# Performance work log

Measured on AMD Instinct MI355X. Metric: run time of the kernel, lower is better.

The kernel has to match this reference:

```python
import jax, jax.numpy as jnp
import numpy as np

N = 100000      # nodes
E = 1600000     # edges (avg degree 16)
F_IN = 128
F_HID = 128
LN_EPS = 1e-5


def setup_inputs() -> dict:
    key = jax.random.key(0)
    ks = jax.random.split(key, 4)
    x = jax.random.normal(ks[0], (N, F_IN), dtype=jnp.float32)
    edge_index = jax.random.randint(ks[1], (2, E), 0, N, dtype=jnp.int32)
    W1 = jax.random.normal(ks[2], (F_IN, F_HID), dtype=jnp.float32) * 0.05
    W2 = jax.random.normal(ks[3], (F_HID, F_HID), dtype=jnp.float32) * 0.05
    return {
        "x": x,
        "edge_index": edge_index,
        "W1": W1, "b1": jnp.zeros((F_HID,), jnp.float32),
        "W2": W2, "b2": jnp.zeros((F_HID,), jnp.float32),
        "g1": jnp.ones((F_HID,), jnp.float32), "be1": jnp.zeros((F_HID,), jnp.float32),
        "g2": jnp.ones((F_HID,), jnp.float32), "be2": jnp.zeros((F_HID,), jnp.float32),
    }


def layer_norm(x, gamma, beta):
    mu = jnp.mean(x, axis=-1, keepdims=True)
    var = jnp.mean(jnp.square(x - mu), axis=-1, keepdims=True)
    return (x - mu) * jax.lax.rsqrt(var + LN_EPS) * gamma + beta


def gcn_conv(x, src, dst, W, b):
    """PyG GCNConv: linear transform, add self-loops, symmetric-normalized scatter-add."""
    n = x.shape[0]
    loop = jnp.arange(n, dtype=src.dtype)
    s = jnp.concatenate([src, loop])   # [E+N] sources (incl. self-loops)
    d = jnp.concatenate([dst, loop])   # [E+N] destinations
    deg = jax.ops.segment_sum(jnp.ones(s.shape[0], x.dtype), d, num_segments=n)
    dinv = jnp.where(deg > 0, jax.lax.rsqrt(deg), 0.0)
    norm = dinv[s] * dinv[d]           # [E+N] edge normalization
    h = x @ W                          # [N, F_hid] transform BEFORE propagate (PyG order)
    msg = h[s] * norm[:, None]         # [E+N, F_hid] gathered, normalized messages
    out = jax.ops.segment_sum(msg, d, num_segments=n)
    return out + b


def reference(x, edge_index, W1, b1, W2, b2, g1, be1, g2, be2):
    # GCN_body, layer=2, layer_norm_first=False, use_ln=True, eval mode (dropout=identity)
    src, dst = edge_index[0], edge_index[1]
    h = layer_norm(jax.nn.relu(gcn_conv(x, src, dst, W1, b1)), g1, be1)
    h = layer_norm(jax.nn.relu(gcn_conv(h, src, dst, W2, b2)), g2, be2)
    return h
```

## Files before the change

### kernel.cpp

```cpp
#include <hip/hip_runtime.h>

#define FDIM 128
#define LN_EPS 1e-5f

typedef short short8 __attribute__((ext_vector_type(8)));
typedef float f32x4 __attribute__((ext_vector_type(4)));

__device__ __forceinline__ ushort f2bf(float f) {
    uint u = __float_as_uint(f);
    u += 0x7fff + ((u >> 16) & 1);
    return (ushort)(u >> 16);
}
__device__ __forceinline__ float bflo(uint u) { return __uint_as_float(u << 16); }
__device__ __forceinline__ float bfhi(uint u) { return __uint_as_float(u & 0xffff0000u); }

__global__ void k_count(const int* __restrict__ dst, int* __restrict__ cnt,
                        ushort* __restrict__ pos, int E) {
    int e = blockIdx.x * 256 + threadIdx.x;
    if (e < E) pos[e] = (ushort)atomicAdd(&cnt[dst[e]], 1);
}

__global__ __launch_bounds__(1024) void k_scan_block(const int* __restrict__ cnt,
                                                     int* __restrict__ rowptr,
                                                     int* __restrict__ partial, int N) {
    __shared__ int s[1024];
    int t = threadIdx.x;
    int i = blockIdx.x * 1024 + t;
    int v = (i < N) ? ((cnt[i] + 7) & ~7) : 0;
    s[t] = v;
    __syncthreads();
    for (int off = 1; off < 1024; off <<= 1) {
        int u = (t >= off) ? s[t - off] : 0;
        __syncthreads();
        s[t] += u;
        __syncthreads();
    }
    if (i < N) rowptr[i] = s[t] - v;
    if (t == 1023) partial[blockIdx.x] = s[1023];
}

__global__ __launch_bounds__(1024) void k_scan_partial(int* __restrict__ partial, int NB) {
    __shared__ int s[1024];
    int t = threadIdx.x;
    int v = (t < NB) ? partial[t] : 0;
    s[t] = v;
    __syncthreads();
    for (int off = 1; off < 1024; off <<= 1) {
        int u = (t >= off) ? s[t - off] : 0;
        __syncthreads();
        s[t] += u;
        __syncthreads();
    }
    if (t < NB) partial[t] = s[t] - v;
}

__global__ void k_finalize(int* __restrict__ rowptr, const int* __restrict__ partial,
                           const int* __restrict__ cnt, float* __restrict__ dinv,
                           int* __restrict__ col, int N, int E) {
    int i = blockIdx.x * 256 + threadIdx.x;
    if (i < N) {
        int rp = rowptr[i] + partial[i >> 10];
        rowptr[i] = rp;
        int deg = cnt[i];
        int deg8 = (deg + 7) & ~7;
        dinv[i] = rsqrtf((float)deg + 1.0f);
        for (int k = deg; k < deg8; ++k) col[rp + k] = N;
        if (i == N - 1) rowptr[N] = rp + deg8;
    }
}

__global__ void k_wt2(const float* __restrict__ W1, const float* __restrict__ W2,
                      ushort* __restrict__ WT1, ushort* __restrict__ WT2) {
    int b = blockIdx.x, k = threadIdx.x;
    if (b < 128) WT1[b * 128 + k] = f2bf(W1[k * 128 + b]);
    else         WT2[(b - 128) * 128 + k] = f2bf(W2[k * 128 + (b - 128)]);
}

template <bool F32IN>
__device__ __forceinline__ void gemm_body(char* sXb, char* sWb,
                                          const void* __restrict__ Xin,
                                          const ushort* __restrict__ WT,
                                          const float* __restrict__ dinv,
                                          ushort* __restrict__ H, int N, int bid) {
    int t = threadIdx.x;
    int w = t >> 6, lane = t & 63;
    int cl = lane & 15, kq = lane >> 4;
    int base = bid * 64;

    const short8* Wg = (const short8*)WT;
#pragma unroll
    for (int k = 0; k < 8; ++k) {
        int idx = t + k * 256;
        int c = idx >> 4, ch = idx & 15;
        *(short8*)(sWb + c * 256 + ((ch * 16) ^ ((c & 7) << 4))) = Wg[idx];
    }

    if constexpr (F32IN) {
        const float4* X4 = (const float4*)Xin;
        size_t lim = (size_t)N * 32 - 1;
#pragma unroll
        for (int k = 0; k < 8; ++k) {
            int idx = t + k * 256;
            size_t gi = (size_t)base * 32 + idx;
            float4 v = X4[gi < lim ? gi : lim];
            ushort4 o;
            o.x = f2bf(v.x); o.y = f2bf(v.y); o.z = f2bf(v.z); o.w = f2bf(v.w);
            int row = idx >> 5, b8 = (idx & 31) * 8;
            *(ushort4*)(sXb + row * 256 + (b8 ^ ((row & 7) << 4))) = o;
        }
    } else {
        const short8* X8 = (const short8*)Xin;
        size_t lim = (size_t)N * 16 - 1;
#pragma unroll
        for (int k = 0; k < 4; ++k) {
            int idx = t + k * 256;
            size_t gi = (size_t)base * 16 + idx;
            short8 v = X8[gi < lim ? gi : lim];
            int row = idx >> 4, b16 = (idx & 15) * 16;
            *(short8*)(sXb + row * 256 + (b16 ^ ((row & 7) << 4))) = v;
        }
    }
    __syncthreads();

    int rl = w * 16 + cl;
    short8 b0, b1, b2, b3;
#pragma unroll
    for (int kt = 0; kt < 4; ++kt) {
        short8 v = *(const short8*)(sXb + rl * 256 + ((kt * 64 + kq * 16) ^ ((rl & 7) << 4)));
        if (kt == 0) b0 = v; else if (kt == 1) b1 = v; else if (kt == 2) b2 = v; else b3 = v;
    }

    int r = base + rl;
    bool ok = r < N;
    float di = dinv[min(r, N - 1)];
#pragma unroll
    for (int nt = 0; nt < 8; ++nt) {
        int c = nt * 16 + cl;
        int sw = (c & 7) << 4;
        f32x4 acc = {0.f, 0.f, 0.f, 0.f};
        acc = __builtin_amdgcn_mfma_f32_16x16x32_bf16(
            *(const short8*)(sWb + c * 256 + ((0 * 64 + kq * 16) ^ sw)), b0, acc, 0, 0, 0);
        acc = __builtin_amdgcn_mfma_f32_16x16x32_bf16(
            *(const short8*)(sWb + c * 256 + ((1 * 64 + kq * 16) ^ sw)), b1, acc, 0, 0, 0);
        acc = __builtin_amdgcn_mfma_f32_16x16x32_bf16(
            *(const short8*)(sWb + c * 256 + ((2 * 64 + kq * 16) ^ sw)), b2, acc, 0, 0, 0);
        acc = __builtin_amdgcn_mfma_f32_16x16x32_bf16(
            *(const short8*)(sWb + c * 256 + ((3 * 64 + kq * 16) ^ sw)), b3, acc, 0, 0, 0);
        if (ok) {
            ushort4 o;
            o.x = f2bf(acc[0] * di); o.y = f2bf(acc[1] * di);
            o.z = f2bf(acc[2] * di); o.w = f2bf(acc[3] * di);
            *(ushort4*)(H + (size_t)r * 128 + nt * 16 + kq * 4) = o;
        }
    }
}

template <bool F32IN>
__global__ __launch_bounds__(256) void k_gemm(const void* __restrict__ Xin,
                                              const ushort* __restrict__ WT,
                                              const float* __restrict__ dinv,
                                              ushort* __restrict__ H, int N) {
    __shared__ ushort sX[64 * 128];
    __shared__ ushort sW[128 * 128];
    gemm_body<F32IN>((char*)sX, (char*)sW, Xin, WT, dinv, H, N, blockIdx.x);
}

__global__ __launch_bounds__(256) void k_mega(const void* __restrict__ Xin,
                                              const ushort* __restrict__ WT,
                                              const float* __restrict__ dinv,
                                              ushort* __restrict__ H, int N, int ngemm,
                                              const int* __restrict__ src,
                                              const int* __restrict__ dst,
                                              const int* __restrict__ rowptr,
                                              const ushort* __restrict__ pos,
                                              int* __restrict__ col, int E) {
    __shared__ ushort sX[64 * 128];
    __shared__ ushort sW[128 * 128];
    if (blockIdx.x < (uint)ngemm) {
        gemm_body<true>((char*)sX, (char*)sW, Xin, WT, dinv, H, N, blockIdx.x);
    } else {
        int e = (blockIdx.x - ngemm) * 256 + threadIdx.x;
        if (e < E) col[rowptr[dst[e]] + (int)pos[e]] = src[e];
    }
}

__global__ __launch_bounds__(256) void k_agg(const uint4* __restrict__ H4,
                                             const int* __restrict__ rowptr,
                                             const int* __restrict__ col,
                                             const float* __restrict__ dinv,
                                             const float* __restrict__ bias,
                                             const float* __restrict__ gamma,
                                             const float* __restrict__ beta,
                                             float* __restrict__ outf,
                                             uint4* __restrict__ outb,
                                             int N) {
    int wave = threadIdx.x >> 6;
    int lane = threadIdx.x & 63;
    int q = lane >> 4;
    int l = lane & 15;
    int node = blockIdx.x * 16 + wave * 4 + q;
    bool valid = node < N;
    int nodec = valid ? node : N - 1;

    float di = dinv[nodec];
    uint4 hs = H4[(uint)nodec * 16u + (uint)l];
    float a0 = bflo(hs.x), a1 = bfhi(hs.x), a2 = bflo(hs.y), a3 = bfhi(hs.y);
    float a4 = bflo(hs.z), a5 = bfhi(hs.z), a6 = bflo(hs.w), a7 = bfhi(hs.w);

    int beg = rowptr[nodec];
    int deg8 = rowptr[nodec + 1] - beg;
    const int* cp = col + beg;

    for (int i = 0; i < deg8; i += 8) {
        int s0 = cp[i + 0], s1 = cp[i + 1], s2 = cp[i + 2], s3 = cp[i + 3];
        int s4 = cp[i + 4], s5 = cp[i + 5], s6 = cp[i + 6], s7 = cp[i + 7];
        uint4 u0 = H4[(uint)s0 * 16u + (uint)l];
        uint4 u1 = H4[(uint)s1 * 16u + (uint)l];
        uint4 u2 = H4[(uint)s2 * 16u + (uint)l];
        uint4 u3 = H4[(uint)s3 * 16u + (uint)l];
        uint4 u4 = H4[(uint)s4 * 16u + (uint)l];
        uint4 u5 = H4[(uint)s5 * 16u + (uint)l];
        uint4 u6 = H4[(uint)s6 * 16u + (uint)l];
        uint4 u7 = H4[(uint)s7 * 16u + (uint)l];
        a0 += bflo(u0.x); a1 += bfhi(u0.x); a2 += bflo(u0.y); a3 += bfhi(u0.y);
        a4 += bflo(u0.z); a5 += bfhi(u0.z); a6 += bflo(u0.w); a7 += bfhi(u0.w);
        a0 += bflo(u1.x); a1 += bfhi(u1.x); a2 += bflo(u1.y); a3 += bfhi(u1.y);
        a4 += bflo(u1.z); a5 += bfhi(u1.z); a6 += bflo(u1.w); a7 += bfhi(u1.w);
        a0 += bflo(u2.x); a1 += bfhi(u2.x); a2 += bflo(u2.y); a3 += bfhi(u2.y);
        a4 += bflo(u2.z); a5 += bfhi(u2.z); a6 += bflo(u2.w); a7 += bfhi(u2.w);
        a0 += bflo(u3.x); a1 += bfhi(u3.x); a2 += bflo(u3.y); a3 += bfhi(u3.y);
        a4 += bflo(u3.z); a5 += bfhi(u3.z); a6 += bflo(u3.w); a7 += bfhi(u3.w);
        a0 += bflo(u4.x); a1 += bfhi(u4.x); a2 += bflo(u4.y); a3 += bfhi(u4.y);
        a4 += bflo(u4.z); a5 += bfhi(u4.z); a6 += bflo(u4.w); a7 += bfhi(u4.w);
        a0 += bflo(u5.x); a1 += bfhi(u5.x); a2 += bflo(u5.y); a3 += bfhi(u5.y);
        a4 += bflo(u5.z); a5 += bfhi(u5.z); a6 += bflo(u5.w); a7 += bfhi(u5.w);
        a0 += bflo(u6.x); a1 += bfhi(u6.x); a2 += bflo(u6.y); a3 += bfhi(u6.y);
        a4 += bflo(u6.z); a5 += bfhi(u6.z); a6 += bflo(u6.w); a7 += bfhi(u6.w);
        a0 += bflo(u7.x); a1 += bfhi(u7.x); a2 += bflo(u7.y); a3 += bfhi(u7.y);
        a4 += bflo(u7.z); a5 += bfhi(u7.z); a6 += bflo(u7.w); a7 += bfhi(u7.w);
    }

    float4 bb0 = ((const float4*)bias)[2 * l];
    float4 bb1 = ((const float4*)bias)[2 * l + 1];
    a0 = fmaxf(fmaf(a0, di, bb0.x), 0.f);
    a1 = fmaxf(fmaf(a1, di, bb0.y), 0.f);
    a2 = fmaxf(fmaf(a2, di, bb0.z), 0.f);
    a3 = fmaxf(fmaf(a3, di, bb0.w), 0.f);
    a4 = fmaxf(fmaf(a4, di, bb1.x), 0.f);
    a5 = fmaxf(fmaf(a5, di, bb1.y), 0.f);
    a6 = fmaxf(fmaf(a6, di, bb1.z), 0.f);
    a7 = fmaxf(fmaf(a7, di, bb1.w), 0.f);

    float s1 = ((a0 + a1) + (a2 + a3)) + ((a4 + a5) + (a6 + a7));
    float s2 = ((a0 * a0 + a1 * a1) + (a2 * a2 + a3 * a3)) +
               ((a4 * a4 + a5 * a5) + (a6 * a6 + a7 * a7));
#pragma unroll
    for (int off = 8; off >= 1; off >>= 1) {
        s1 += __shfl_xor(s1, off);
        s2 += __shfl_xor(s2, off);
    }
    float mu = s1 * (1.f / 128.f);
    float var = s2 * (1.f / 128.f) - mu * mu;
    float rs = rsqrtf(var + LN_EPS);

    float4 g0 = ((const float4*)gamma)[2 * l];
    float4 g1 = ((const float4*)gamma)[2 * l + 1];
    float4 e0 = ((const float4*)beta)[2 * l];
    float4 e1 = ((const float4*)beta)[2 * l + 1];
    float o0 = (a0 - mu) * rs * g0.x + e0.x;
    float o1 = (a1 - mu) * rs * g0.y + e0.y;
    float o2 = (a2 - mu) * rs * g0.z + e0.z;
    float o3 = (a3 - mu) * rs * g0.w + e0.w;
    float o4 = (a4 - mu) * rs * g1.x + e1.x;
    float o5 = (a5 - mu) * rs * g1.y + e1.y;
    float o6 = (a6 - mu) * rs * g1.z + e1.z;
    float o7 = (a7 - mu) * rs * g1.w + e1.w;

    if (!valid) return;
    if (outf) {
        ((float4*)outf)[(size_t)node * 32 + 2 * l]     = make_float4(o0, o1, o2, o3);
        ((float4*)outf)[(size_t)node * 32 + 2 * l + 1] = make_float4(o4, o5, o6, o7);
    } else {
        uint4 o;
        o.x = (uint)f2bf(o0) | ((uint)f2bf(o1) << 16);
        o.y = (uint)f2bf(o2) | ((uint)f2bf(o3) << 16);
        o.z = (uint)f2bf(o4) | ((uint)f2bf(o5) << 16);
        o.w = (uint)f2bf(o6) | ((uint)f2bf(o7) << 16);
        outb[(size_t)node * 16 + l] = o;
    }
}

extern "C" void kernel_launch(void* const* d_in, const int* in_sizes, int n_in,
                              void* d_out, int out_size, void* d_ws, size_t ws_size,
                              hipStream_t stream) {
    const float* x  = (const float*)d_in[0];
    const int*   ei = (const int*)d_in[1];
    const float* W1 = (const float*)d_in[2];
    const float* b1 = (const float*)d_in[3];
    const float* W2 = (const float*)d_in[4];
    const float* b2 = (const float*)d_in[5];
    const float* g1 = (const float*)d_in[6];
    const float* be1 = (const float*)d_in[7];
    const float* g2 = (const float*)d_in[8];
    const float* be2 = (const float*)d_in[9];

    int N = in_sizes[0] / FDIM;
    int E = in_sizes[1] / 2;
    const int* srcp = ei;
    const int* dstp = ei + E;
    float* out = (float*)d_out;

    char* w = (char*)d_ws;
    size_t off = 0;
    auto take = [&](size_t bytes) {
        void* p = w + off;
        off = (off + bytes + 255) & ~(size_t)255;
        return p;
    };
    ushort* hb   = (ushort*)take((size_t)(N + 1) * FDIM * sizeof(ushort));
    ushort* WT1  = (ushort*)take(128 * 128 * sizeof(ushort));
    ushort* WT2  = (ushort*)take(128 * 128 * sizeof(ushort));
    int* cnt     = (int*)take((size_t)N * sizeof(int));
    int* rowptr  = (int*)take((size_t)(N + 1) * sizeof(int));
    ushort* pos  = (ushort*)take((size_t)E * sizeof(ushort));
    int* colb    = (int*)take((size_t)(E + 7 * (size_t)N + 8) * sizeof(int));
    float* dinv  = (float*)take((size_t)N * sizeof(float));
    int* partial = (int*)take(1024 * sizeof(int));
    (void)ws_size;

    int NB = (N + 1023) >> 10;
    int ngemm = (N + 63) / 64;
    int nfill = (E + 255) / 256;

    hipMemsetAsync(cnt, 0, (size_t)N * sizeof(int), stream);
    hipMemsetAsync(hb + (size_t)N * FDIM, 0, FDIM * sizeof(ushort), stream);

    k_wt2<<<256, 128, 0, stream>>>(W1, W2, WT1, WT2);

    k_count<<<(E + 255) / 256, 256, 0, stream>>>(dstp, cnt, pos, E);
    k_scan_block<<<NB, 1024, 0, stream>>>(cnt, rowptr, partial, N);
    k_scan_partial<<<1, 1024, 0, stream>>>(partial, NB);
    k_finalize<<<(N + 255) / 256, 256, 0, stream>>>(rowptr, partial, cnt, dinv, colb, N, E);

    k_mega<<<ngemm + nfill, 256, 0, stream>>>(x, WT1, dinv, hb, N, ngemm,
                                              srcp, dstp, rowptr, pos, colb, E);

    k_agg<<<(N + 15) / 16, 256, 0, stream>>>((const uint4*)hb, rowptr, colb, dinv,
                                             b1, g1, be1, nullptr, (uint4*)d_out, N);
    k_gemm<false><<<ngemm, 256, 0, stream>>>(d_out, WT2, dinv, hb, N);
    k_agg<<<(N + 15) / 16, 256, 0, stream>>>((const uint4*)hb, rowptr, colb, dinv,
                                             b2, g2, be2, out, nullptr, N);
}
```

Before: 260.6 us.

## Privatize degree counting per XCD to avoid cross-die atomic contention

```diff
diff --git a/kernel.cpp b/kernel.cpp
--- a/kernel.cpp
+++ b/kernel.cpp
@@ -2,6 +2,7 @@
 
 #define FDIM 128
 #define LN_EPS 1e-5f
+#define NXCD 8
 
 typedef short short8 __attribute__((ext_vector_type(8)));
 typedef float f32x4 __attribute__((ext_vector_type(4)));
@@ -14,19 +15,36 @@
 __device__ __forceinline__ float bflo(uint u) { return __uint_as_float(u << 16); }
 __device__ __forceinline__ float bfhi(uint u) { return __uint_as_float(u & 0xffff0000u); }
 
-__global__ void k_count(const int* __restrict__ dst, int* __restrict__ cnt,
-                        ushort* __restrict__ pos, int E) {
+__device__ __forceinline__ uint xcc_id() {
+    uint x;
+    asm volatile("s_getreg_b32 %0, hwreg(20, 0, 32)" : "=s"(x));
+    return x & (NXCD - 1);
+}
+
+__global__ void k_count(const int* __restrict__ dst, uint* __restrict__ partial,
+                        ushort* __restrict__ pos, int N, int E) {
     int e = blockIdx.x * 256 + threadIdx.x;
-    if (e < E) pos[e] = (ushort)atomicAdd(&cnt[dst[e]], 1);
-}
-
-__global__ __launch_bounds__(1024) void k_scan_block(const int* __restrict__ cnt,
+    uint x = xcc_id();
+    if (e < E) {
+        uint slot = __hip_atomic_fetch_add(&partial[(size_t)x * N + dst[e]], 1u,
+                                           __ATOMIC_RELAXED, __HIP_MEMORY_SCOPE_WORKGROUP);
+        pos[e] = (ushort)((x << 13) | (slot & 0x1FFFu));
+    }
+}
+
+__global__ __launch_bounds__(1024) void k_scan_block(const uint* __restrict__ partial,
                                                      int* __restrict__ rowptr,
-                                                     int* __restrict__ partial, int N) {
+                                                     int* __restrict__ partialscan, int N) {
     __shared__ int s[1024];
     int t = threadIdx.x;
     int i = blockIdx.x * 1024 + t;
-    int v = (i < N) ? ((cnt[i] + 7) & ~7) : 0;
+    int v = 0;
+    if (i < N) {
+        int deg = 0;
+#pragma unroll
+        for (int x = 0; x < NXCD; ++x) deg += (int)partial[(size_t)x * N + i];
+        v = (deg + 7) & ~7;
+    }
     s[t] = v;
     __syncthreads();
     for (int off = 1; off < 1024; off <<= 1) {
@@ -36,13 +54,13 @@
         __syncthreads();
     }
     if (i < N) rowptr[i] = s[t] - v;
-    if (t == 1023) partial[blockIdx.x] = s[1023];
-}
-
-__global__ __launch_bounds__(1024) void k_scan_partial(int* __restrict__ partial, int NB) {
+    if (t == 1023) partialscan[blockIdx.x] = s[1023];
+}
+
+__global__ __launch_bounds__(1024) void k_scan_partial(int* __restrict__ partialscan, int NB) {
     __shared__ int s[1024];
     int t = threadIdx.x;
-    int v = (t < NB) ? partial[t] : 0;
+    int v = (t < NB) ? partialscan[t] : 0;
     s[t] = v;
     __syncthreads();
     for (int off = 1; off < 1024; off <<= 1) {
@@ -51,17 +69,24 @@
         s[t] += u;
         __syncthreads();
     }
-    if (t < NB) partial[t] = s[t] - v;
-}
-
-__global__ void k_finalize(int* __restrict__ rowptr, const int* __restrict__ partial,
-                           const int* __restrict__ cnt, float* __restrict__ dinv,
+    if (t < NB) partialscan[t] = s[t] - v;
+}
+
+__global__ void k_finalize(int* __restrict__ rowptr, const int* __restrict__ partialscan,
+                           uint* __restrict__ partial, float* __restrict__ dinv,
                            int* __restrict__ col, int N, int E) {
     int i = blockIdx.x * 256 + threadIdx.x;
     if (i < N) {
-        int rp = rowptr[i] + partial[i >> 10];
+        int rp = rowptr[i] + partialscan[i >> 10];
         rowptr[i] = rp;
-        int deg = cnt[i];
+        int run = rp, deg = 0;
+#pragma unroll
+        for (int x = 0; x < NXCD; ++x) {
+            uint c = partial[(size_t)x * N + i];
+            partial[(size_t)x * N + i] = (uint)run;
+            run += (int)c;
+            deg += (int)c;
+        }
         int deg8 = (deg + 7) & ~7;
         dinv[i] = rsqrtf((float)deg + 1.0f);
         for (int k = deg; k < deg8; ++k) col[rp + k] = N;
@@ -171,7 +196,7 @@
                                               ushort* __restrict__ H, int N, int ngemm,
                                               const int* __restrict__ src,
                                               const int* __restrict__ dst,
-                                              const int* __restrict__ rowptr,
+                                              const uint* __restrict__ basep,
                                               const ushort* __restrict__ pos,
                                               int* __restrict__ col, int E) {
     __shared__ ushort sX[64 * 128];
@@ -180,7 +205,12 @@
         gemm_body<true>((char*)sX, (char*)sW, Xin, WT, dinv, H, N, blockIdx.x);
     } else {
         int e = (blockIdx.x - ngemm) * 256 + threadIdx.x;
-        if (e < E) col[rowptr[dst[e]] + (int)pos[e]] = src[e];
+        if (e < E) {
+            int d = dst[e];
+            uint u = pos[e];
+            uint x = u >> 13, p = u & 0x1FFFu;
+            col[basep[(size_t)x * N + d] + p] = src[e];
+        }
     }
 }
 
@@ -317,33 +347,33 @@
         off = (off + bytes + 255) & ~(size_t)255;
         return p;
     };
-    ushort* hb   = (ushort*)take((size_t)(N + 1) * FDIM * sizeof(ushort));
-    ushort* WT1  = (ushort*)take(128 * 128 * sizeof(ushort));
-    ushort* WT2  = (ushort*)take(128 * 128 * sizeof(ushort));
-    int* cnt     = (int*)take((size_t)N * sizeof(int));
-    int* rowptr  = (int*)take((size_t)(N + 1) * sizeof(int));
-    ushort* pos  = (ushort*)take((size_t)E * sizeof(ushort));
-    int* colb    = (int*)take((size_t)(E + 7 * (size_t)N + 8) * sizeof(int));
-    float* dinv  = (float*)take((size_t)N * sizeof(float));
-    int* partial = (int*)take(1024 * sizeof(int));
+    ushort* hb    = (ushort*)take((size_t)(N + 1) * FDIM * sizeof(ushort));
+    ushort* WT1   = (ushort*)take(128 * 128 * sizeof(ushort));
+    ushort* WT2   = (ushort*)take(128 * 128 * sizeof(ushort));
+    uint* partial = (uint*)take((size_t)NXCD * N * sizeof(uint));
+    int* rowptr   = (int*)take((size_t)(N + 1) * sizeof(int));
+    ushort* pos   = (ushort*)take((size_t)E * sizeof(ushort));
+    int* colb     = (int*)take((size_t)(E + 7 * (size_t)N + 1024) * sizeof(int));
+    float* dinv   = (float*)take((size_t)N * sizeof(float));
+    int* pscan    = (int*)take(1024 * sizeof(int));
     (void)ws_size;
 
     int NB = (N + 1023) >> 10;
     int ngemm = (N + 63) / 64;
     int nfill = (E + 255) / 256;
 
-    hipMemsetAsync(cnt, 0, (size_t)N * sizeof(int), stream);
+    hipMemsetAsync(partial, 0, (size_t)NXCD * N * sizeof(uint), stream);
     hipMemsetAsync(hb + (size_t)N * FDIM, 0, FDIM * sizeof(ushort), stream);
 
     k_wt2<<<256, 128, 0, stream>>>(W1, W2, WT1, WT2);
 
-    k_count<<<(E + 255) / 256, 256, 0, stream>>>(dstp, cnt, pos, E);
-    k_scan_block<<<NB, 1024, 0, stream>>>(cnt, rowptr, partial, N);
-    k_scan_partial<<<1, 1024, 0, stream>>>(partial, NB);
-    k_finalize<<<(N + 255) / 256, 256, 0, stream>>>(rowptr, partial, cnt, dinv, colb, N, E);
+    k_count<<<(E + 255) / 256, 256, 0, stream>>>(dstp, partial, pos, N, E);
+    k_scan_block<<<NB, 1024, 0, stream>>>(partial, rowptr, pscan, N);
+    k_scan_partial<<<1, 1024, 0, stream>>>(pscan, NB);
+    k_finalize<<<(N + 255) / 256, 256, 0, stream>>>(rowptr, pscan, partial, dinv, colb, N, E);
 
     k_mega<<<ngemm + nfill, 256, 0, stream>>>(x, WT1, dinv, hb, N, ngemm,
-                                              srcp, dstp, rowptr, pos, colb, E);
+                                              srcp, dstp, partial, pos, colb, E);
 
     k_agg<<<(N + 15) / 16, 256, 0, stream>>>((const uint4*)hb, rowptr, colb, dinv,
                                              b1, g1, be1, nullptr, (uint4*)d_out, N);
```

New measurement: 260.5 us. About the same (-0.0%).

## Build CSR with two-level bucketed radix scatter instead of global atomics

Applied to the files above, without the earlier changes.

```diff
diff --git a/kernel.cpp b/kernel.cpp
--- a/kernel.cpp
+++ b/kernel.cpp
@@ -2,6 +2,8 @@
 
 #define FDIM 128
 #define LN_EPS 1e-5f
+#define BSH 9
+#define EPB 2048
 
 typedef short short8 __attribute__((ext_vector_type(8)));
 typedef float f32x4 __attribute__((ext_vector_type(4)));
@@ -14,58 +16,175 @@
 __device__ __forceinline__ float bflo(uint u) { return __uint_as_float(u << 16); }
 __device__ __forceinline__ float bfhi(uint u) { return __uint_as_float(u & 0xffff0000u); }
 
-__global__ void k_count(const int* __restrict__ dst, int* __restrict__ cnt,
-                        ushort* __restrict__ pos, int E) {
-    int e = blockIdx.x * 256 + threadIdx.x;
-    if (e < E) pos[e] = (ushort)atomicAdd(&cnt[dst[e]], 1);
-}
-
-__global__ __launch_bounds__(1024) void k_scan_block(const int* __restrict__ cnt,
-                                                     int* __restrict__ rowptr,
-                                                     int* __restrict__ partial, int N) {
-    __shared__ int s[1024];
+
+__global__ __launch_bounds__(256) void k_bcount(const int* __restrict__ dst,
+                                                uint* __restrict__ mat, int nbk, int E) {
+    __shared__ uint cnt[512];
     int t = threadIdx.x;
-    int i = blockIdx.x * 1024 + t;
-    int v = (i < N) ? ((cnt[i] + 7) & ~7) : 0;
-    s[t] = v;
-    __syncthreads();
-    for (int off = 1; off < 1024; off <<= 1) {
-        int u = (t >= off) ? s[t - off] : 0;
-        __syncthreads();
-        s[t] += u;
-        __syncthreads();
-    }
-    if (i < N) rowptr[i] = s[t] - v;
-    if (t == 1023) partial[blockIdx.x] = s[1023];
-}
-
-__global__ __launch_bounds__(1024) void k_scan_partial(int* __restrict__ partial, int NB) {
-    __shared__ int s[1024];
+    for (int i = t; i < nbk; i += 256) cnt[i] = 0;
+    __syncthreads();
+    int base = blockIdx.x * EPB, end = min(base + EPB, E);
+    for (int e = base + t; e < end; e += 256)
+        atomicAdd(&cnt[(uint)dst[e] >> BSH], 1u);
+    __syncthreads();
+    for (int i = t; i < nbk; i += 256) mat[(size_t)blockIdx.x * nbk + i] = cnt[i];
+}
+
+__global__ __launch_bounds__(1024) void k_colscan(uint* __restrict__ mat,
+                                                  uint* __restrict__ btot, int nbk, int nblk) {
+    __shared__ uint s[1024];
+    int b = blockIdx.x, t = threadIdx.x;
+    uint run = 0;
+    for (int base = 0; base < nblk; base += 1024) {
+        int i = base + t;
+        uint v = (i < nblk) ? mat[(size_t)i * nbk + b] : 0;
+        s[t] = v;
+        __syncthreads();
+        for (int off = 1; off < 1024; off <<= 1) {
+            uint u = (t >= off) ? s[t - off] : 0;
+            __syncthreads();
+            s[t] += u;
+            __syncthreads();
+        }
+        if (i < nblk) mat[(size_t)i * nbk + b] = run + s[t] - v;
+        run += s[1023];
+        __syncthreads();
+    }
+    if (t == 0) btot[b] = run;
+}
+
+__global__ __launch_bounds__(256) void k_bscatter(const int* __restrict__ src,
+                                                  const int* __restrict__ dst,
+                                                  const uint* __restrict__ mat,
+                                                  const uint* __restrict__ btot,
+                                                  uint* __restrict__ ebuf, int nbk, int E) {
+    __shared__ uint cur[512];
+    __shared__ uint ps[256];
     int t = threadIdx.x;
-    int v = (t < NB) ? partial[t] : 0;
-    s[t] = v;
-    __syncthreads();
-    for (int off = 1; off < 1024; off <<= 1) {
-        int u = (t >= off) ? s[t - off] : 0;
-        __syncthreads();
-        s[t] += u;
-        __syncthreads();
-    }
-    if (t < NB) partial[t] = s[t] - v;
-}
-
-__global__ void k_finalize(int* __restrict__ rowptr, const int* __restrict__ partial,
-                           const int* __restrict__ cnt, float* __restrict__ dinv,
-                           int* __restrict__ col, int N, int E) {
-    int i = blockIdx.x * 256 + threadIdx.x;
-    if (i < N) {
-        int rp = rowptr[i] + partial[i >> 10];
-        rowptr[i] = rp;
-        int deg = cnt[i];
-        int deg8 = (deg + 7) & ~7;
-        dinv[i] = rsqrtf((float)deg + 1.0f);
-        for (int k = deg; k < deg8; ++k) col[rp + k] = N;
-        if (i == N - 1) rowptr[N] = rp + deg8;
+    uint v = (t < nbk) ? btot[t] : 0;
+    ps[t] = v;
+    __syncthreads();
+    for (int off = 1; off < 256; off <<= 1) {
+        uint u = (t >= off) ? ps[t - off] : 0;
+        __syncthreads();
+        ps[t] += u;
+        __syncthreads();
+    }
+    if (t < nbk) cur[t] = (ps[t] - v) + mat[(size_t)blockIdx.x * nbk + t];
+    __syncthreads();
+    int base = blockIdx.x * EPB, end = min(base + EPB, E);
+    for (int e = base + t; e < end; e += 256) {
+        uint d = (uint)dst[e];
+        uint off = atomicAdd(&cur[d >> BSH], 1u);
+        ebuf[off] = ((d & 511u) << 17) | (uint)src[e];
+    }
+}
+
+__global__ __launch_bounds__(256) void k_bdeg(const uint* __restrict__ ebuf,
+                                              const uint* __restrict__ btot,
+                                              int* __restrict__ deg, float* __restrict__ dinv,
+                                              uint* __restrict__ padtot, int N, int nbk) {
+    __shared__ uint cnt[512];
+    __shared__ uint ps[256];
+    __shared__ uint begs;
+    int b = blockIdx.x, t = threadIdx.x;
+    for (int i = t; i < 512; i += 256) cnt[i] = 0;
+    uint v = (t < nbk) ? btot[t] : 0;
+    ps[t] = v;
+    __syncthreads();
+    for (int off = 1; off < 256; off <<= 1) {
+        uint u = (t >= off) ? ps[t - off] : 0;
+        __syncthreads();
+        ps[t] += u;
+        __syncthreads();
+    }
+    if (t == b) begs = ps[t] - v;
+    __syncthreads();
+    uint beg = begs, cn = btot[b];
+    for (uint i = t; i < cn; i += 256) atomicAdd(&cnt[ebuf[beg + i] >> 17], 1u);
+    __syncthreads();
+    int n0 = b << BSH;
+    uint loc = 0;
+    for (int i = t; i < 512; i += 256) {
+        int n = n0 + i;
+        if (n < N) {
+            uint dg = cnt[i];
+            deg[n] = (int)dg;
+            dinv[n] = rsqrtf((float)dg + 1.0f);
+            loc += (dg + 7u) & ~7u;
+        }
+    }
+    ps[t] = loc;
+    __syncthreads();
+    for (int off = 128; off >= 1; off >>= 1) {
+        if (t < off) ps[t] += ps[t + off];
+        __syncthreads();
+    }
+    if (t == 0) padtot[b] = ps[0];
+}
+
+__device__ __forceinline__ void bfill_body(const uint* __restrict__ ebuf,
+                                           const uint* __restrict__ btot,
+                                           const uint* __restrict__ padtot,
+                                           const int* __restrict__ deg,
+                                           int* __restrict__ rowptr, int* __restrict__ col,
+                                           int N, int nbk, int b) {
+    __shared__ uint ps[256];
+    __shared__ uint lrp[512];
+    __shared__ uint curf[512];
+    __shared__ uint sc0, sc1;
+    int t = threadIdx.x;
+    uint v = (t < nbk) ? btot[t] : 0;
+    ps[t] = v;
+    __syncthreads();
+    for (int off = 1; off < 256; off <<= 1) {
+        uint u = (t >= off) ? ps[t - off] : 0;
+        __syncthreads();
+        ps[t] += u;
+        __syncthreads();
+    }
+    if (t == b) sc0 = ps[t] - v;
+    __syncthreads();
+    uint w = (t < nbk) ? padtot[t] : 0;
+    ps[t] = w;
+    __syncthreads();
+    for (int off = 1; off < 256; off <<= 1) {
+        uint u = (t >= off) ? ps[t - off] : 0;
+        __syncthreads();
+        ps[t] += u;
+        __syncthreads();
+    }
+    if (t == b) sc1 = ps[t] - w;
+    if (b == nbk - 1 && t == nbk - 1) rowptr[N] = (int)ps[t];
+    __syncthreads();
+    uint beg = sc0, cn = btot[b], base = sc1;
+    int n0 = b << BSH;
+    int nA = n0 + 2 * t, nB = nA + 1;
+    uint dA = (nA < N) ? (uint)deg[nA] : 0;
+    uint dB = (nB < N) ? (uint)deg[nB] : 0;
+    uint pA = (dA + 7u) & ~7u, pB = (dB + 7u) & ~7u;
+    uint pair = pA + pB;
+    ps[t] = pair;
+    __syncthreads();
+    for (int off = 1; off < 256; off <<= 1) {
+        uint u = (t >= off) ? ps[t - off] : 0;
+        __syncthreads();
+        ps[t] += u;
+        __syncthreads();
+    }
+    uint pex = ps[t] - pair;
+    uint rA = base + pex, rB = rA + pA;
+    lrp[2 * t] = rA; lrp[2 * t + 1] = rB;
+    curf[2 * t] = rA; curf[2 * t + 1] = rB;
+    if (nA < N) rowptr[nA] = (int)rA;
+    if (nB < N) rowptr[nB] = (int)rB;
+    if (nA < N) for (uint k = dA; k < pA; ++k) col[rA + k] = N;
+    if (nB < N) for (uint k = dB; k < pB; ++k) col[rB + k] = N;
+    __syncthreads();
+    for (uint i = t; i < cn; i += 256) {
+        uint e = ebuf[beg + i];
+        uint p = atomicAdd(&curf[e >> 17], 1u);
+        col[p] = (int)(e & 0x1FFFFu);
     }
 }
 
@@ -169,18 +288,18 @@
                                               const ushort* __restrict__ WT,
                                               const float* __restrict__ dinv,
                                               ushort* __restrict__ H, int N, int ngemm,
-                                              const int* __restrict__ src,
-                                              const int* __restrict__ dst,
-                                              const int* __restrict__ rowptr,
-                                              const ushort* __restrict__ pos,
-                                              int* __restrict__ col, int E) {
+                                              const uint* __restrict__ ebuf,
+                                              const uint* __restrict__ btot,
+                                              const uint* __restrict__ padtot,
+                                              const int* __restrict__ deg,
+                                              int* __restrict__ rowptr,
+                                              int* __restrict__ col, int nbk) {
     __shared__ ushort sX[64 * 128];
     __shared__ ushort sW[128 * 128];
     if (blockIdx.x < (uint)ngemm) {
         gemm_body<true>((char*)sX, (char*)sW, Xin, WT, dinv, H, N, blockIdx.x);
     } else {
-        int e = (blockIdx.x - ngemm) * 256 + threadIdx.x;
-        if (e < E) col[rowptr[dst[e]] + (int)pos[e]] = src[e];
+        bfill_body(ebuf, btot, padtot, deg, rowptr, col, N, nbk, blockIdx.x - ngemm);
     }
 }
 
@@ -317,33 +436,35 @@
         off = (off + bytes + 255) & ~(size_t)255;
         return p;
     };
+    int nbk  = (N + 511) >> BSH;
+    int nblk = (E + EPB - 1) / EPB;
+
     ushort* hb   = (ushort*)take((size_t)(N + 1) * FDIM * sizeof(ushort));
     ushort* WT1  = (ushort*)take(128 * 128 * sizeof(ushort));
     ushort* WT2  = (ushort*)take(128 * 128 * sizeof(ushort));
-    int* cnt     = (int*)take((size_t)N * sizeof(int));
+    uint* mat    = (uint*)take((size_t)nblk * nbk * sizeof(uint));
+    uint* btot   = (uint*)take((size_t)nbk * sizeof(uint));
+    uint* padtot = (uint*)take((size_t)nbk * sizeof(uint));
+    uint* ebuf   = (uint*)take((size_t)E * sizeof(uint));
+    int* deg     = (int*)take((size_t)N * sizeof(int));
     int* rowptr  = (int*)take((size_t)(N + 1) * sizeof(int));
-    ushort* pos  = (ushort*)take((size_t)E * sizeof(ushort));
-    int* colb    = (int*)take((size_t)(E + 7 * (size_t)N + 8) * sizeof(int));
+    int* colb    = (int*)take((size_t)(E + 7 * (size_t)N + 1024) * sizeof(int));
     float* dinv  = (float*)take((size_t)N * sizeof(float));
-    int* partial = (int*)take(1024 * sizeof(int));
     (void)ws_size;
 
-    int NB = (N + 1023) >> 10;
     int ngemm = (N + 63) / 64;
-    int nfill = (E + 255) / 256;
-
-    hipMemsetAsync(cnt, 0, (size_t)N * sizeof(int), stream);
+
     hipMemsetAsync(hb + (size_t)N * FDIM, 0, FDIM * sizeof(ushort), stream);
 
     k_wt2<<<256, 128, 0, stream>>>(W1, W2, WT1, WT2);
 
-    k_count<<<(E + 255) / 256, 256, 0, stream>>>(dstp, cnt, pos, E);
-    k_scan_block<<<NB, 1024, 0, stream>>>(cnt, rowptr, partial, N);
-    k_scan_partial<<<1, 1024, 0, stream>>>(partial, NB);
-    k_finalize<<<(N + 255) / 256, 256, 0, stream>>>(rowptr, partial, cnt, dinv, colb, N, E);
-
-    k_mega<<<ngemm + nfill, 256, 0, stream>>>(x, WT1, dinv, hb, N, ngemm,
-                                              srcp, dstp, rowptr, pos, colb, E);
+    k_bcount<<<nblk, 256, 0, stream>>>(dstp, mat, nbk, E);
+    k_colscan<<<nbk, 1024, 0, stream>>>(mat, btot, nbk, nblk);
+    k_bscatter<<<nblk, 256, 0, stream>>>(srcp, dstp, mat, btot, ebuf, nbk, E);
+    k_bdeg<<<nbk, 256, 0, stream>>>(ebuf, btot, deg, dinv, padtot, N, nbk);
+
+    k_mega<<<ngemm + nbk, 256, 0, stream>>>(x, WT1, dinv, hb, N, ngemm,
+                                            ebuf, btot, padtot, deg, rowptr, colb, nbk);
 
     k_agg<<<(N + 15) / 16, 256, 0, stream>>>((const uint4*)hb, rowptr, colb, dinv,
                                              b1, g1, be1, nullptr, (uint4*)d_out, N);
```

Result: faster. 221.7 us (-14.9%).
